# Kernel tuning notes

Measured on AMD Instinct MI355X. Metric: run time of the kernel, lower is better.

The kernel has to match this reference:

```python
import jax, jax.numpy as jnp
import numpy as np

N_NODES = 16384
N_EDGES = 32768
D = 128          # node feature / hidden dim
EDGE_DIM = 10    # bond featurizer one-hot dim
EH = 32          # edge_hidden_dim in the NNConv MLPs


def _nnconv(x, src, dst, edge_attr, l1w, l1b, l2w, l2b, root, bias):
    """PyG NNConv with aggr='mean': out_i = x_i @ root + mean_{e: dst=i} x_{src_e} @ W(e) + bias."""
    E = edge_attr.shape[0]
    h = jax.nn.relu(edge_attr @ l1w + l1b)              # [E, EH]
    W = (h @ l2w + l2b).reshape(E, D, D)                # per-edge weight matrices [E, D, D]
    msg = jnp.einsum('ei,eio->eo', x[src], W)           # gather + per-edge matmul [E, D]
    s = jax.ops.segment_sum(msg, dst, num_segments=N_NODES)
    cnt = jax.ops.segment_sum(jnp.ones((E, 1), x.dtype), dst, num_segments=N_NODES)
    agg = s / jnp.maximum(cnt, 1.0)                     # scatter-mean (0 for isolated nodes)
    return x @ root + agg + bias


def setup_inputs() -> dict:
    key = jax.random.key(0)
    ks = jax.random.split(key, 14)
    x = jax.random.normal(ks[0], (N_NODES, D), dtype=jnp.float32)
    edge_index = jax.random.randint(ks[1], (2, N_EDGES), 0, N_NODES, dtype=jnp.int64)
    edge_attr = jax.random.uniform(ks[2], (N_EDGES, EDGE_DIM), dtype=jnp.float32)

    def lin(k, fan_in, fan_out):
        return jax.random.normal(k, (fan_in, fan_out), dtype=jnp.float32) / np.sqrt(fan_in)

    return {
        'x': x, 'edge_index': edge_index, 'edge_attr': edge_attr,
        # subgraph_conv1 (128 -> 128)
        'w1_l1': lin(ks[3], EDGE_DIM, EH), 'b1_l1': jnp.zeros((EH,), jnp.float32),
        'w1_l2': lin(ks[4], EH, D * D),    'b1_l2': jnp.zeros((D * D,), jnp.float32),
        'w1_root': lin(ks[5], D, D),       'b1': jnp.zeros((D,), jnp.float32),
        # subgraph_conv2 (128 -> 128), applied twice with shared weights
        'w2_l1': lin(ks[6], EDGE_DIM, EH), 'b2_l1': jnp.zeros((EH,), jnp.float32),
        'w2_l2': lin(ks[7], EH, D * D),    'b2_l2': jnp.zeros((D * D,), jnp.float32),
        'w2_root': lin(ks[8], D, D),       'b2': jnp.zeros((D,), jnp.float32),
    }


def reference(x, edge_index, edge_attr,
              w1_l1, b1_l1, w1_l2, b1_l2, w1_root, b1,
              w2_l1, b2_l1, w2_l2, b2_l2, w2_root, b2):
    src, dst = edge_index[0], edge_index[1]
    h = jax.nn.relu(_nnconv(x, src, dst, edge_attr, w1_l1, b1_l1, w1_l2, b1_l2, w1_root, b1))
    h = jax.nn.relu(_nnconv(h, src, dst, edge_attr, w2_l1, b2_l1, w2_l2, b2_l2, w2_root, b2))
    h = _nnconv(h, src, dst, edge_attr, w2_l1, b2_l1, w2_l2, b2_l2, w2_root, b2)
    return h
```

## Files before the change

kernel.cpp:

```cpp
#include <hip/hip_runtime.h>

#define N_NODES 16384
#define N_EDGES 32768
#define D 128
#define EDGE_DIM 10
#define KH 32
#define BM 128
#define XST2 72
#define XST 136
#define NBL 32

typedef _Float16 f16;
typedef _Float16 f16x4 __attribute__((ext_vector_type(4)));
typedef _Float16 f16x8 __attribute__((ext_vector_type(8)));
typedef float f32x4 __attribute__((ext_vector_type(4)));

__global__ __launch_bounds__(256) void deg_pack_kernel(
    const int* __restrict__ ei, int* __restrict__ deg,
    const float* __restrict__ w1l2, const float* __restrict__ w2l2,
    const float* __restrict__ b1l2, const float* __restrict__ b2l2,
    const float* __restrict__ rt1, const float* __restrict__ rt2,
    f16* __restrict__ Bp1, f16* __restrict__ Bp2,
    f16* __restrict__ Rp1, f16* __restrict__ Rp2) {
  int y = blockIdx.y;
  if (y == 0) {
    int e = blockIdx.x * 256 + threadIdx.x;
    if (e < N_EDGES) atomicAdd(&deg[ei[N_EDGES + e]], 1);
    return;
  }
  if (blockIdx.x >= D * D / 256) return;
  int t = blockIdx.x * 256 + threadIdx.x;
  int j = y - 1;
  if (j < 2) {
    const float* l2w = j ? w2l2 : w1l2;
    f16* Bp = j ? Bp2 : Bp1;
    f16 tmp[KH];
#pragma unroll
    for (int k = 0; k < KH; k++) tmp[k] = (f16)l2w[(size_t)k * (D * D) + t];
    f16x8* dst = (f16x8*)(Bp + (size_t)t * KH);
#pragma unroll
    for (int c = 0; c < 4; c++) dst[c] = *(f16x8*)&tmp[c * 8];
  } else {
    const float* src = (j == 2) ? b1l2 : (j == 3) ? b2l2 : (j == 4) ? rt1 : rt2;
    f16* dst = (j == 2) ? (Bp1 + (size_t)D * D * KH)
             : (j == 3) ? (Bp2 + (size_t)D * D * KH)
             : (j == 4) ? Rp1 : Rp2;
    int i = t >> 7, o = t & 127;
    dst[((size_t)(i >> 5) * D + o) * KH + (i & 31)] = (f16)src[t];
  }
}

__global__ __launch_bounds__(1024) void scan_kernel(
    const int* __restrict__ deg, int* __restrict__ rs, int* __restrict__ fill) {
  __shared__ int part[1024];
  int t = threadIdx.x;
  int base = t * 16;
  int loc[16], s = 0;
#pragma unroll
  for (int j = 0; j < 16; j++) { loc[j] = deg[base + j]; s += loc[j]; }
  part[t] = s;
  __syncthreads();
  for (int off = 1; off < 1024; off <<= 1) {
    int add = (t >= off) ? part[t - off] : 0;
    __syncthreads();
    part[t] += add;
    __syncthreads();
  }
  int run = t ? part[t - 1] : 0;
#pragma unroll
  for (int j = 0; j < 16; j++) {
    rs[base + j] = run; fill[base + j] = run; run += loc[j];
  }
  if (t == 1023) rs[N_NODES] = run;
}

__global__ __launch_bounds__(256) void scatter_kernel(
    const int* __restrict__ ei, int* __restrict__ fill,
    int* __restrict__ perm, int* __restrict__ srcs) {
  int e = blockIdx.x * blockDim.x + threadIdx.x;
  if (e < N_EDGES) {
    int pos = atomicAdd(&fill[ei[N_EDGES + e]], 1);
    perm[pos] = e;
    srcs[pos] = ei[e];
  }
}

__global__ __launch_bounds__(256) void edge_mlp_kernel(
    const float* __restrict__ ea, const int* __restrict__ perm,
    const float* __restrict__ w1l1, const float* __restrict__ b1l1,
    const float* __restrict__ w2l1, const float* __restrict__ b2l1,
    f16* __restrict__ h1, f16* __restrict__ h2) {
  int p = blockIdx.x * blockDim.x + threadIdx.x;
  const float* l1w = blockIdx.y ? w2l1 : w1l1;
  const float* l1b = blockIdx.y ? b2l1 : b1l1;
  f16* h = blockIdx.y ? h2 : h1;
  int e = perm[p];
  float a[EDGE_DIM];
#pragma unroll
  for (int d = 0; d < EDGE_DIM; d++) a[d] = ea[e * EDGE_DIM + d];
  f16 hv[KH];
#pragma unroll
  for (int k = 0; k < KH; k++) {
    float acc = l1b[k];
#pragma unroll
    for (int d = 0; d < EDGE_DIM; d++) acc += a[d] * l1w[d * KH + k];
    hv[k] = (f16)fmaxf(acc, 0.0f);
  }
  f16x8* dst = (f16x8*)(h + (size_t)p * KH);
#pragma unroll
  for (int c = 0; c < 4; c++) dst[c] = *(f16x8*)&hv[c * 8];
}

__global__ __launch_bounds__(256, 2) void msg_mfma_kernel(
    const float* __restrict__ xin, const f16* __restrict__ hf,
    const f16* __restrict__ Bp, const int* __restrict__ srcs,
    f16* __restrict__ msgfA, f16* __restrict__ msgfB) {
  __shared__ f16 Xs[BM][XST2];
  __shared__ f16 Hs[BM][KH];
  int t = threadIdx.x;
  int e0 = blockIdx.x * BM;
  int y  = blockIdx.y;
  f16* msgf = y ? msgfB : msgfA;

  ((f16x8*)Hs)[t]       = ((const f16x8*)(hf + (size_t)e0 * KH))[t];
  ((f16x8*)Hs)[t + 256] = ((const f16x8*)(hf + (size_t)e0 * KH))[t + 256];
  {
    int r = t >> 1, q = t & 1;
    int s = srcs[e0 + r];
    const float4* src = (const float4*)(xin + (size_t)s * D + y * 64 + q * 32);
    f16* dst = &Xs[r][q * 32];
#pragma unroll
    for (int c = 0; c < 8; c++) {
      float4 v = src[c];
      f16x4 h4 = {(f16)v.x, (f16)v.y, (f16)v.z, (f16)v.w};
      *(f16x4*)(dst + c * 4) = h4;
    }
  }

  int L = t & 63, w = t >> 6;
  int quad = L >> 4, lm = L & 15;
  int n0 = w * 32;

  const f16* bl = Bp + ((size_t)(y * 64) * D + n0 + lm) * KH + quad * 8;
  const size_t istr = (size_t)D * KH;

  f32x4 acc[8][2];
#pragma unroll
  for (int mt = 0; mt < 8; mt++)
#pragma unroll
    for (int nt = 0; nt < 2; nt++)
      acc[mt][nt] = (f32x4){0.f, 0.f, 0.f, 0.f};

  f16x8 bufA[4][2], bufB[4][2];

  auto loadg = [&](f16x8 (&buf)[4][2], int basei) {
#pragma unroll
    for (int jj = 0; jj < 4; jj++) {
      const f16* bi = bl + (size_t)(basei + jj) * istr;
      buf[jj][0] = *(const f16x8*)bi;
      buf[jj][1] = *(const f16x8*)(bi + 16 * KH);
    }
  };

  f16x8 hreg[8];

  auto compute = [&](f16x8 (&buf)[4][2], int ig) {
    f16x4 xv[8];
#pragma unroll
    for (int mt = 0; mt < 8; mt++)
      xv[mt] = *(const f16x4*)&Xs[mt * 16 + lm][ig];
#pragma unroll
    for (int jj = 0; jj < 4; jj++) {
#pragma unroll
      for (int mt = 0; mt < 8; mt++) {
        f16 xs = xv[mt][jj];
        f16x8 xb = {xs, xs, xs, xs, xs, xs, xs, xs};
        f16x8 a = hreg[mt] * xb;
        acc[mt][0] = __builtin_amdgcn_mfma_f32_16x16x32_f16(a, buf[jj][0], acc[mt][0], 0, 0, 0);
        acc[mt][1] = __builtin_amdgcn_mfma_f32_16x16x32_f16(a, buf[jj][1], acc[mt][1], 0, 0, 0);
      }
    }
  };

  loadg(bufA, 0);
  __syncthreads();

#pragma unroll
  for (int mt = 0; mt < 8; mt++)
    hreg[mt] = *(const f16x8*)&Hs[mt * 16 + lm][quad * 8];

#pragma unroll 1
  for (int g = 0; g < 8; g++) {
    loadg(bufB, 8 * g + 4);
    compute(bufA, 8 * g);
    loadg(bufA, 8 * g + 8);
    compute(bufB, 8 * g + 4);
  }

  {
    const f16* bb = Bp + (size_t)D * D * KH;
#pragma unroll
    for (int g2 = 0; g2 < 2; g2++) {
      int ig2 = 2 * y + g2;
      const f16* b2l = bb + ((size_t)ig2 * D + n0 + lm) * KH + quad * 8;
      f16x8 b0 = *(const f16x8*)b2l;
      f16x8 b1 = *(const f16x8*)(b2l + 16 * KH);
      int lc = g2 * 32 + quad * 8;
#pragma unroll
      for (int mt = 0; mt < 8; mt++) {
        f16x8 a = *(const f16x8*)&Xs[mt * 16 + lm][lc];
        acc[mt][0] = __builtin_amdgcn_mfma_f32_16x16x32_f16(a, b0, acc[mt][0], 0, 0, 0);
        acc[mt][1] = __builtin_amdgcn_mfma_f32_16x16x32_f16(a, b1, acc[mt][1], 0, 0, 0);
      }
    }
  }

#pragma unroll
  for (int mt = 0; mt < 8; mt++)
#pragma unroll
    for (int r = 0; r < 4; r++) {
      f16* mg = msgf + (size_t)(e0 + mt * 16 + quad * 4 + r) * D + n0 + lm;
      mg[0]  = (f16)acc[mt][0][r];
      mg[16] = (f16)acc[mt][1][r];
    }
}

__global__ __launch_bounds__(256) void node_update_kernel(
    const float* __restrict__ xin, const f16* __restrict__ msgA,
    const f16* __restrict__ msgB, const int* __restrict__ rs,
    const f16* __restrict__ Rp, const float* __restrict__ bias,
    float* __restrict__ out, int do_relu) {
  __shared__ f16 Xs[NBL][XST];
  __shared__ float Sls[NBL][D];
  int t = threadIdx.x;
  int nb = blockIdx.x * NBL;

  {
    int r = t >> 3, q = t & 7;
    const float4* src = (const float4*)(xin + (size_t)(nb + r) * D + q * 16);
    f16* dst = &Xs[r][q * 16];
#pragma unroll
    for (int c = 0; c < 4; c++) {
      float4 v = src[c];
      f16x4 h4 = {(f16)v.x, (f16)v.y, (f16)v.z, (f16)v.w};
      *(f16x4*)(dst + c * 4) = h4;
    }
  }
  __syncthreads();

  {
    int nl = t >> 3, o0 = (t & 7) * 16;
    int n = nb + nl;
    int a = rs[n], b = rs[n + 1];
    float sum[16];
#pragma unroll
    for (int j = 0; j < 16; j++) sum[j] = 0.f;
    for (int r = a; r < b; r++) {
      f16x8 a0 = *(const f16x8*)(msgA + (size_t)r * D + o0);
      f16x8 a1 = *(const f16x8*)(msgA + (size_t)r * D + o0 + 8);
      f16x8 b0 = *(const f16x8*)(msgB + (size_t)r * D + o0);
      f16x8 b1 = *(const f16x8*)(msgB + (size_t)r * D + o0 + 8);
#pragma unroll
      for (int j = 0; j < 8; j++) {
        sum[j]     += (float)a0[j] + (float)b0[j];
        sum[8 + j] += (float)a1[j] + (float)b1[j];
      }
    }
    float inv = 1.0f / (float)max(b - a, 1);
#pragma unroll
    for (int j = 0; j < 16; j++) Sls[nl][o0 + j] = sum[j] * inv;
  }
  __syncthreads();

  int L = t & 63, w = t >> 6;
  int quad = L >> 4, lm = L & 15;
  int n0 = w * 32;
  f32x4 acc[2][2];
#pragma unroll
  for (int mt = 0; mt < 2; mt++)
#pragma unroll
    for (int nt = 0; nt < 2; nt++)
      acc[mt][nt] = (f32x4){0.f, 0.f, 0.f, 0.f};
#pragma unroll
  for (int s4 = 0; s4 < 4; s4++) {
    const f16* b2l = Rp + ((size_t)s4 * D + n0 + lm) * KH + quad * 8;
    f16x8 b0 = *(const f16x8*)b2l;
    f16x8 b1 = *(const f16x8*)(b2l + 16 * KH);
#pragma unroll
    for (int mt = 0; mt < 2; mt++) {
      f16x8 a = *(const f16x8*)&Xs[mt * 16 + lm][s4 * 32 + quad * 8];
      acc[mt][0] = __builtin_amdgcn_mfma_f32_16x16x32_f16(a, b0, acc[mt][0], 0, 0, 0);
      acc[mt][1] = __builtin_amdgcn_mfma_f32_16x16x32_f16(a, b1, acc[mt][1], 0, 0, 0);
    }
  }
#pragma unroll
  for (int mt = 0; mt < 2; mt++)
#pragma unroll
    for (int r = 0; r < 4; r++) {
      Sls[mt * 16 + quad * 4 + r][n0 + lm] += acc[mt][0][r];
      Sls[mt * 16 + quad * 4 + r][n0 + 16 + lm] += acc[mt][1][r];
    }
  __syncthreads();

  {
    int o = t & 127, g = t >> 7;
    float bo = bias[o];
    for (int q = g * 16; q < g * 16 + 16; q++) {
      float v = bo + Sls[q][o];
      out[(size_t)(nb + q) * D + o] = do_relu ? fmaxf(v, 0.0f) : v;
    }
  }
}

extern "C" void kernel_launch(void* const* d_in, const int* in_sizes, int n_in,
                              void* d_out, int out_size, void* d_ws, size_t ws_size,
                              hipStream_t stream) {
  const float* x      = (const float*)d_in[0];
  const int*   ei     = (const int*)d_in[1];
  const float* ea     = (const float*)d_in[2];
  const float* w1_l1  = (const float*)d_in[3];
  const float* b1_l1  = (const float*)d_in[4];
  const float* w1_l2  = (const float*)d_in[5];
  const float* b1_l2  = (const float*)d_in[6];
  const float* w1_rt  = (const float*)d_in[7];
  const float* b1     = (const float*)d_in[8];
  const float* w2_l1  = (const float*)d_in[9];
  const float* b2_l1  = (const float*)d_in[10];
  const float* w2_l2  = (const float*)d_in[11];
  const float* b2_l2  = (const float*)d_in[12];
  const float* w2_rt  = (const float*)d_in[13];
  const float* b2     = (const float*)d_in[14];
  float* out = (float*)d_out;

  const size_t BPSZ = (size_t)D * D * KH + (size_t)D * D + 32768;
  f16* h1f = (f16*)d_ws;
  f16* h2f = h1f + (size_t)N_EDGES * KH;
  f16* Bp1 = h2f + (size_t)N_EDGES * KH;
  f16* Bp2 = Bp1 + BPSZ;
  f16* Rp1 = Bp2 + BPSZ;
  f16* Rp2 = Rp1 + (size_t)D * D;
  int* deg  = (int*)(Rp2 + (size_t)D * D);
  int* rs   = deg + N_NODES;
  int* fill = rs + N_NODES + 128;
  int* perm = fill + N_NODES;
  int* srcs = perm + N_EDGES;
  f16* msgA = (f16*)(srcs + N_EDGES);
  f16* msgB = msgA + (size_t)N_EDGES * D;

  hipMemsetAsync(deg, 0, N_NODES * sizeof(int), stream);
  deg_pack_kernel<<<dim3(N_EDGES / 256, 7), 256, 0, stream>>>(
      ei, deg, w1_l2, w2_l2, b1_l2, b2_l2, w1_rt, w2_rt, Bp1, Bp2, Rp1, Rp2);
  scan_kernel<<<1, 1024, 0, stream>>>(deg, rs, fill);
  scatter_kernel<<<N_EDGES / 256, 256, 0, stream>>>(ei, fill, perm, srcs);
  edge_mlp_kernel<<<dim3(N_EDGES / 256, 2), 256, 0, stream>>>(
      ea, perm, w1_l1, b1_l1, w2_l1, b2_l1, h1f, h2f);

  msg_mfma_kernel<<<dim3(N_EDGES / BM, 2), 256, 0, stream>>>(x, h1f, Bp1, srcs, msgA, msgB);
  node_update_kernel<<<N_NODES / NBL, 256, 0, stream>>>(x, msgA, msgB, rs, Rp1, b1, out, 1);
  msg_mfma_kernel<<<dim3(N_EDGES / BM, 2), 256, 0, stream>>>(out, h2f, Bp2, srcs, msgA, msgB);
  node_update_kernel<<<N_NODES / NBL, 256, 0, stream>>>(out, msgA, msgB, rs, Rp2, b2, out, 1);
  msg_mfma_kernel<<<dim3(N_EDGES / BM, 2), 256, 0, stream>>>(out, h2f, Bp2, srcs, msgA, msgB);
  node_update_kernel<<<N_NODES / NBL, 256, 0, stream>>>(out, msgA, msgB, rs, Rp2, b2, out, 0);
}
```

Measured before the change: 235.5 us.

## Process full input dim per block with smaller edge tile, drop split-K partials

The message kernel used to split the 128-wide input dimension across two grid columns, each writing a partial fp16 message buffer that the node update then summed. Now each block covers all 128 input features for 64 edges, so a single message buffer is written and read. This halves message-buffer traffic and removes the second partial sum. In exchange, each block streams the full per-edge weight basis for only half as many edges, which lowers B reuse. Summing in fp32 inside the MFMA accumulator rather than across two fp16 partials also changes rounding slightly.

```diff
diff --git a/kernel.cpp b/kernel.cpp
--- a/kernel.cpp
+++ b/kernel.cpp
@@ -5,8 +5,8 @@
 #define D 128
 #define EDGE_DIM 10
 #define KH 32
-#define BM 128
-#define XST2 72
+#define BM 64
+#define XMS 136
 #define XST 136
 #define NBL 32
 
@@ -114,20 +114,17 @@
 __global__ __launch_bounds__(256, 2) void msg_mfma_kernel(
     const float* __restrict__ xin, const f16* __restrict__ hf,
     const f16* __restrict__ Bp, const int* __restrict__ srcs,
-    f16* __restrict__ msgfA, f16* __restrict__ msgfB) {
-  __shared__ f16 Xs[BM][XST2];
+    f16* __restrict__ msgf) {
+  __shared__ f16 Xs[BM][XMS];
   __shared__ f16 Hs[BM][KH];
   int t = threadIdx.x;
   int e0 = blockIdx.x * BM;
-  int y  = blockIdx.y;
-  f16* msgf = y ? msgfB : msgfA;
-
-  ((f16x8*)Hs)[t]       = ((const f16x8*)(hf + (size_t)e0 * KH))[t];
-  ((f16x8*)Hs)[t + 256] = ((const f16x8*)(hf + (size_t)e0 * KH))[t + 256];
-  {
-    int r = t >> 1, q = t & 1;
+
+  ((f16x8*)Hs)[t] = ((const f16x8*)(hf + (size_t)e0 * KH))[t];
+  {
+    int r = t >> 2, q = t & 3;
     int s = srcs[e0 + r];
-    const float4* src = (const float4*)(xin + (size_t)s * D + y * 64 + q * 32);
+    const float4* src = (const float4*)(xin + (size_t)s * D + q * 32);
     f16* dst = &Xs[r][q * 32];
 #pragma unroll
     for (int c = 0; c < 8; c++) {
@@ -141,12 +138,12 @@
   int quad = L >> 4, lm = L & 15;
   int n0 = w * 32;
 
-  const f16* bl = Bp + ((size_t)(y * 64) * D + n0 + lm) * KH + quad * 8;
+  const f16* bl = Bp + ((size_t)(n0 + lm)) * KH + quad * 8;
   const size_t istr = (size_t)D * KH;
 
-  f32x4 acc[8][2];
-#pragma unroll
-  for (int mt = 0; mt < 8; mt++)
+  f32x4 acc[4][2];
+#pragma unroll
+  for (int mt = 0; mt < 4; mt++)
 #pragma unroll
     for (int nt = 0; nt < 2; nt++)
       acc[mt][nt] = (f32x4){0.f, 0.f, 0.f, 0.f};
@@ -162,17 +159,17 @@
     }
   };
 
-  f16x8 hreg[8];
+  f16x8 hreg[4];
 
   auto compute = [&](f16x8 (&buf)[4][2], int ig) {
-    f16x4 xv[8];
-#pragma unroll
-    for (int mt = 0; mt < 8; mt++)
+    f16x4 xv[4];
+#pragma unroll
+    for (int mt = 0; mt < 4; mt++)
       xv[mt] = *(const f16x4*)&Xs[mt * 16 + lm][ig];
 #pragma unroll
     for (int jj = 0; jj < 4; jj++) {
 #pragma unroll
-      for (int mt = 0; mt < 8; mt++) {
+      for (int mt = 0; mt < 4; mt++) {
         f16 xs = xv[mt][jj];
         f16x8 xb = {xs, xs, xs, xs, xs, xs, xs, xs};
         f16x8 a = hreg[mt] * xb;
@@ -186,11 +183,11 @@
   __syncthreads();
 
 #pragma unroll
-  for (int mt = 0; mt < 8; mt++)
+  for (int mt = 0; mt < 4; mt++)
     hreg[mt] = *(const f16x8*)&Hs[mt * 16 + lm][quad * 8];
 
 #pragma unroll 1
-  for (int g = 0; g < 8; g++) {
+  for (int g = 0; g < 16; g++) {
     loadg(bufB, 8 * g + 4);
     compute(bufA, 8 * g);
     loadg(bufA, 8 * g + 8);
@@ -200,14 +197,13 @@
   {
     const f16* bb = Bp + (size_t)D * D * KH;
 #pragma unroll
-    for (int g2 = 0; g2 < 2; g2++) {
-      int ig2 = 2 * y + g2;
-      const f16* b2l = bb + ((size_t)ig2 * D + n0 + lm) * KH + quad * 8;
+    for (int g2 = 0; g2 < 4; g2++) {
+      const f16* b2l = bb + ((size_t)g2 * D + n0 + lm) * KH + quad * 8;
       f16x8 b0 = *(const f16x8*)b2l;
       f16x8 b1 = *(const f16x8*)(b2l + 16 * KH);
       int lc = g2 * 32 + quad * 8;
 #pragma unroll
-      for (int mt = 0; mt < 8; mt++) {
+      for (int mt = 0; mt < 4; mt++) {
         f16x8 a = *(const f16x8*)&Xs[mt * 16 + lm][lc];
         acc[mt][0] = __builtin_amdgcn_mfma_f32_16x16x32_f16(a, b0, acc[mt][0], 0, 0, 0);
         acc[mt][1] = __builtin_amdgcn_mfma_f32_16x16x32_f16(a, b1, acc[mt][1], 0, 0, 0);
@@ -216,7 +212,7 @@
   }
 
 #pragma unroll
-  for (int mt = 0; mt < 8; mt++)
+  for (int mt = 0; mt < 4; mt++)
 #pragma unroll
     for (int r = 0; r < 4; r++) {
       f16* mg = msgf + (size_t)(e0 + mt * 16 + quad * 4 + r) * D + n0 + lm;
@@ -226,10 +222,9 @@
 }
 
 __global__ __launch_bounds__(256) void node_update_kernel(
-    const float* __restrict__ xin, const f16* __restrict__ msgA,
-    const f16* __restrict__ msgB, const int* __restrict__ rs,
-    const f16* __restrict__ Rp, const float* __restrict__ bias,
-    float* __restrict__ out, int do_relu) {
+    const float* __restrict__ xin, const f16* __restrict__ msg,
+    const int* __restrict__ rs, const f16* __restrict__ Rp,
+    const float* __restrict__ bias, float* __restrict__ out, int do_relu) {
   __shared__ f16 Xs[NBL][XST];
   __shared__ float Sls[NBL][D];
   int t = threadIdx.x;
@@ -256,14 +251,12 @@
 #pragma unroll
     for (int j = 0; j < 16; j++) sum[j] = 0.f;
     for (int r = a; r < b; r++) {
-      f16x8 a0 = *(const f16x8*)(msgA + (size_t)r * D + o0);
-      f16x8 a1 = *(const f16x8*)(msgA + (size_t)r * D + o0 + 8);
-      f16x8 b0 = *(const f16x8*)(msgB + (size_t)r * D + o0);
-      f16x8 b1 = *(const f16x8*)(msgB + (size_t)r * D + o0 + 8);
+      f16x8 a0 = *(const f16x8*)(msg + (size_t)r * D + o0);
+      f16x8 a1 = *(const f16x8*)(msg + (size_t)r * D + o0 + 8);
 #pragma unroll
       for (int j = 0; j < 8; j++) {
-        sum[j]     += (float)a0[j] + (float)b0[j];
-        sum[8 + j] += (float)a1[j] + (float)b1[j];
+        sum[j]     += (float)a0[j];
+        sum[8 + j] += (float)a1[j];
       }
     }
     float inv = 1.0f / (float)max(b - a, 1);
@@ -344,8 +337,7 @@
   int* fill = rs + N_NODES + 128;
   int* perm = fill + N_NODES;
   int* srcs = perm + N_EDGES;
-  f16* msgA = (f16*)(srcs + N_EDGES);
-  f16* msgB = msgA + (size_t)N_EDGES * D;
+  f16* msg  = (f16*)(srcs + N_EDGES);
 
   hipMemsetAsync(deg, 0, N_NODES * sizeof(int), stream);
   deg_pack_kernel<<<dim3(N_EDGES / 256, 7), 256, 0, stream>>>(
@@ -355,10 +347,10 @@
   edge_mlp_kernel<<<dim3(N_EDGES / 256, 2), 256, 0, stream>>>(
       ea, perm, w1_l1, b1_l1, w2_l1, b2_l1, h1f, h2f);
 
-  msg_mfma_kernel<<<dim3(N_EDGES / BM, 2), 256, 0, stream>>>(x, h1f, Bp1, srcs, msgA, msgB);
-  node_update_kernel<<<N_NODES / NBL, 256, 0, stream>>>(x, msgA, msgB, rs, Rp1, b1, out, 1);
-  msg_mfma_kernel<<<dim3(N_EDGES / BM, 2), 256, 0, stream>>>(out, h2f, Bp2, srcs, msgA, msgB);
-  node_update_kernel<<<N_NODES / NBL, 256, 0, stream>>>(out, msgA, msgB, rs, Rp2, b2, out, 1);
-  msg_mfma_kernel<<<dim3(N_EDGES / BM, 2), 256, 0, stream>>>(out, h2f, Bp2, srcs, msgA, msgB);
-  node_update_kernel<<<N_NODES / NBL, 256, 0, stream>>>(out, msgA, msgB, rs, Rp2, b2, out, 0);
-}
+  msg_mfma_kernel<<<N_EDGES / BM, 256, 0, stream>>>(x, h1f, Bp1, srcs, msg);
+  node_update_kernel<<<N_NODES / NBL, 256, 0, stream>>>(x, msg, rs, Rp1, b1, out, 1);
+  msg_mfma_kernel<<<N_EDGES / BM, 256, 0, stream>>>(out, h2f, Bp2, srcs, msg);
+  node_update_kernel<<<N_NODES / NBL, 256, 0, stream>>>(out, msg, rs, Rp2, b2, out, 1);
+  msg_mfma_kernel<<<N_EDGES / BM, 256, 0, stream>>>(out, h2f, Bp2, srcs, msg);
+  node_update_kernel<<<N_NODES / NBL, 256, 0, stream>>>(out, msg, rs, Rp2, b2, out, 0);
+}
```

Result: slower. 261.9 us (+11.2%).
